# Kernel tuning notes

Measured on AMD Instinct MI355X. Metric: run time of the kernel, lower is better.

Reference implementation:

```python
import jax, jax.numpy as jnp
import numpy as np
from math import sqrt

B, H, L, E = 2, 16, 1024, 64
MEM, LMEM = 896, 128
KV = L + MEM + LMEM  # 2048


def rel_shift(x):
    # Transformer-XL relative shift. x: [B,H,i,j] -> [B,H,i,j]
    b, h, i, j = x.shape
    x = jnp.pad(x, ((0, 0), (0, 0), (0, 0), (0, i)))  # [B,H,i,i+j]
    l = i + j - 1
    x = x.reshape(b, h, -1)
    pad = (-x.shape[-1]) % l
    x = jnp.pad(x, ((0, 0), (0, 0), (0, pad))).reshape(b, h, -1, l)
    return x[..., :i, i - 1:]


def setup_inputs() -> dict:
    key = jax.random.key(0)
    kq, kk, kv_, kp = jax.random.split(key, 4)
    return {
        "q": jax.random.normal(kq, (B, H, L, E), jnp.float32),
        "k": jax.random.normal(kk, (B, H, KV, E), jnp.float32),
        "v": jax.random.normal(kv_, (B, H, KV, E), jnp.float32),
        "attn_mask": jnp.ones((B, L), bool),
        "pos_emb": jax.random.normal(kp, (H, KV, E), jnp.float32),
        "kv_len": KV,
        "mem_len": MEM,
        "lmem_len": LMEM,
    }


def reference(q, k, v, attn_mask, pos_emb, kv_len, mem_len, lmem_len):
    b, h, l, e = q.shape
    scale = 1.0 / sqrt(e)
    dots = jnp.einsum('bhid,bhjd->bhij', q, k) * scale  # [B,H,L,KV]
    mask_value = -jnp.finfo(dots.dtype).max

    # relative position bias
    pos = pos_emb[:, -kv_len:].astype(q.dtype)  # [H,KV,E]
    pos_dots = jnp.einsum('bhid,hjd->bhij', q, pos) * scale
    pos_dots = rel_shift(pos_dots)
    left = dots.shape[-1] - pos_dots.shape[-1]
    pos_dots = jnp.pad(pos_dots, ((0, 0), (0, 0), (0, 0), (left, 0)))
    dots = dots + pos_dots

    total_mem = mem_len + lmem_len
    # padding mask
    m = attn_mask[:, None, :, None] & attn_mask[:, None, None, :]  # [B,1,L,L]
    m = jnp.pad(m, ((0, 0), (0, 0), (0, 0), (total_mem, 0)), constant_values=True)
    dots = jnp.where(m, dots, mask_value)
    # causal mask (memory positions always visible)
    causal = jnp.triu(jnp.ones((l, l + total_mem), bool), k=1 + total_mem)
    dots = jnp.where(causal[None, None], mask_value, dots)

    attn = jax.nn.softmax(dots, axis=-1)  # dropout in eval mode -> identity
    out = jnp.einsum('bhij,bhjd->bhid', attn, v)
    return out.transpose(0, 2, 1, 3).reshape(b, l, h * e)
```

## Files before the change

kernel.cpp:

```cpp
#include <hip/hip_runtime.h>
#include <stdint.h>


typedef __attribute__((ext_vector_type(4))) float f32x4;
typedef __attribute__((ext_vector_type(8))) short s16x8;
typedef __attribute__((ext_vector_type(2))) unsigned int u32x2;
typedef unsigned short ushort_t;

#define L_Q 1024
#define NKV 2048
#define TM  1024
#define NPOS 2176

#define WS_K   0
#define WS_VT  4194304
#define WS_POS 8388608
#define WS_TOTAL_USHORT 10616832
#define WS_NEED_BYTES (WS_TOTAL_USHORT * 2)

#define QS_CONST (0.125f * 1.44269504088896340736f)
#define M_FIXED 8.0f

__device__ __forceinline__ void mfma16(f32x4& c, s16x8 a, s16x8 b) {
  asm("v_mfma_f32_16x16x32_bf16 %0, %1, %2, %0" : "+v"(c) : "v"(a), "v"(b));
}

__device__ __forceinline__ float exp2_(float x) {
#if __has_builtin(__builtin_amdgcn_exp2f)
  return __builtin_amdgcn_exp2f(x);
#else
  float r; asm("v_exp_f32 %0, %1" : "=v"(r) : "v"(x)); return r;
#endif
}

__device__ __forceinline__ ushort_t f2bf(float f) {
  union { float f; unsigned int u; } v; v.f = f;
  unsigned int u = v.u;
  return (ushort_t)((u + 0x7FFFu + ((u >> 16) & 1u)) >> 16);
}

__device__ __forceinline__ void gl_lds16(const ushort_t* g, ushort_t* l) {
  __builtin_amdgcn_global_load_lds(
      (const __attribute__((address_space(1))) unsigned int*)g,
      (__attribute__((address_space(3))) unsigned int*)l, 16, 0, 0);
}

__device__ __forceinline__ s16x8 ldfrag(const ushort_t* base, int row, int chunk) {
  int idx = (row * 64 + chunk * 8) ^ ((row & 7) << 3);
  return *(const s16x8*)(base + idx);
}


#define NK_U 524288
#define NP_U 278528
#define LIN_TOTAL 802816

__global__ __launch_bounds__(256) void prep_lin(
    const float* __restrict__ k, const float* __restrict__ pos,
    ushort_t* __restrict__ ws)
{
  int u = blockIdx.x * 256 + threadIdx.x;
  if (u >= LIN_TOTAL) return;
  if (u < NK_U) {
    int bh = u >> 14, rem = u & 16383;
    int j = rem >> 3, db = (rem & 7) << 3;
    size_t off = (((size_t)(bh << 11) + j) << 6);
    f32x4 a = *(const f32x4*)(k + off + db);
    f32x4 b = *(const f32x4*)(k + off + db + 4);
    s16x8 o;
    o[0] = (short)f2bf(a[0]); o[1] = (short)f2bf(a[1]);
    o[2] = (short)f2bf(a[2]); o[3] = (short)f2bf(a[3]);
    o[4] = (short)f2bf(b[0]); o[5] = (short)f2bf(b[1]);
    o[6] = (short)f2bf(b[2]); o[7] = (short)f2bf(b[3]);
    *(s16x8*)(ws + WS_K + off + (db ^ ((j & 7) << 3))) = o;
  } else {
    int t = u - NK_U;
    int h = t / 17408;
    int rem = t - h * 17408;
    int p = rem >> 3, db = (rem & 7) << 3;
    s16x8 o;
    if (p < 2048) {
      size_t off = (((size_t)(h << 11) + p) << 6) + db;
      f32x4 a = *(const f32x4*)(pos + off);
      f32x4 b = *(const f32x4*)(pos + off + 4);
      o[0] = (short)f2bf(a[0]); o[1] = (short)f2bf(a[1]);
      o[2] = (short)f2bf(a[2]); o[3] = (short)f2bf(a[3]);
      o[4] = (short)f2bf(b[0]); o[5] = (short)f2bf(b[1]);
      o[6] = (short)f2bf(b[2]); o[7] = (short)f2bf(b[3]);
    } else {
      for (int e = 0; e < 8; ++e) o[e] = 0;
    }
    *(s16x8*)(ws + WS_POS + (size_t)h * (NPOS * 64) + p * 64 + (db ^ ((p & 7) << 3))) = o;
  }
}

__global__ __launch_bounds__(256) void prep_vt(
    const float* __restrict__ v, ushort_t* __restrict__ ws)
{
  int u = blockIdx.x * 256 + threadIdx.x;
  int bh = u >> 12, rem = u & 4095;
  int tile = rem >> 7, r2 = rem & 127;
  int jl = r2 >> 3, db = (r2 & 7) << 3;
  int j0 = tile << 6;
  ushort_t vals[4][8];
#pragma unroll
  for (int m = 0; m < 4; ++m) {
    size_t off = (((size_t)(bh << 11) + j0 + jl + 16 * m) << 6) + db;
    f32x4 a = *(const f32x4*)(v + off);
    f32x4 b = *(const f32x4*)(v + off + 4);
    vals[m][0] = f2bf(a[0]); vals[m][1] = f2bf(a[1]);
    vals[m][2] = f2bf(a[2]); vals[m][3] = f2bf(a[3]);
    vals[m][4] = f2bf(b[0]); vals[m][5] = f2bf(b[1]);
    vals[m][6] = f2bf(b[2]); vals[m][7] = f2bf(b[3]);
  }
  ushort_t* vt = ws + WS_VT;
#pragma unroll
  for (int e = 0; e < 8; ++e) {
    int d = db + e;
    int cpos = (jl << 2) ^ ((d & 7) << 3);
    union { ushort_t s[4]; u32x2 w; } pk;
    pk.s[0] = vals[0][e]; pk.s[1] = vals[1][e];
    pk.s[2] = vals[2][e]; pk.s[3] = vals[3][e];
    *(u32x2*)(vt + (((size_t)(bh << 6) + d) << 11) + j0 + cpos) = pk.w;
  }
}


__global__ __launch_bounds__(256, 2) void memattn_fast(
    const float* __restrict__ q, const ushort_t* __restrict__ ws,
    float* __restrict__ out)
{
  __shared__ __align__(16) ushort_t sK[2][64 * 64];
  __shared__ __align__(16) ushort_t sV[2][64 * 64];
  __shared__ __align__(16) ushort_t sPos[2][128 * 64];
  __shared__ __align__(16) ushort_t sPl[4 * 16 * 72];

  const int tid = threadIdx.x;
  const int lane = tid & 63;
  const int w = tid >> 6;
  const int bid = blockIdx.x;
  const int bh = bid & 31;
  const int raw = bid >> 5;
  const int ib = (raw < 8) ? raw : 23 - raw;
  const int h = bh & 15;
  const int b = bh >> 4;
  const int i0 = ib * 64;
  const int iw0 = i0 + w * 16;
  const int jc = lane & 15;
  const int g = lane >> 4;

  const ushort_t* kb = ws + WS_K + (size_t)bh * (NKV * 64);
  const ushort_t* vtb = ws + WS_VT + (size_t)bh * (64 * NKV);
  const ushort_t* pb = ws + WS_POS + (size_t)h * (NPOS * 64);

  s16x8 qf[2];
  {
    const float* qr = q + (size_t)bh * (L_Q * 64) + (size_t)(iw0 + jc) * 64 + g * 8;
#pragma unroll
    for (int c = 0; c < 2; ++c) {
      f32x4 a = *(const f32x4*)(qr + 32 * c);
      f32x4 b2 = *(const f32x4*)(qr + 32 * c + 4);
      s16x8 f;
      f[0] = (short)f2bf(a[0] * QS_CONST); f[1] = (short)f2bf(a[1] * QS_CONST);
      f[2] = (short)f2bf(a[2] * QS_CONST); f[3] = (short)f2bf(a[3] * QS_CONST);
      f[4] = (short)f2bf(b2[0] * QS_CONST); f[5] = (short)f2bf(b2[1] * QS_CONST);
      f[6] = (short)f2bf(b2[2] * QS_CONST); f[7] = (short)f2bf(b2[3] * QS_CONST);
      qf[c] = f;
    }
  }

  f32x4 l4, acc[4];
#pragma unroll
  for (int r = 0; r < 4; ++r) l4[r] = 0.f;
#pragma unroll
  for (int d = 0; d < 4; ++d) { f32x4 z = {0.f, 0.f, 0.f, 0.f}; acc[d] = z; }

  int srcl[4]; int lof[4];
#pragma unroll
  for (int reg = 0; reg < 4; ++reg) {
    int r = 4 * g + reg;
    int sc = jc + 15 - r;
    srcl[reg] = (lane & 48) | (sc & 15);
    lof[reg] = (sc < 16);
  }

  const int nsteps = ib + 17;
  const int lrow8 = lane >> 3;
  const int lc8 = (lane & 7) * 8;

  auto STAGE = [&](int buf, int st) {
    const int j0 = st * 64;
    const int pwb = j0 - i0 + 960;
#pragma unroll
    for (int c2 = 0; c2 < 2; ++c2) {
      int c = 2 * w + c2;
      gl_lds16(kb + (size_t)(j0 + c * 8 + lrow8) * 64 + lc8, &sK[buf][c * 512]);
    }
#pragma unroll
    for (int c2 = 0; c2 < 2; ++c2) {
      int c = 2 * w + c2;
      gl_lds16(vtb + (size_t)(c * 8 + lrow8) * NKV + j0 + lc8, &sV[buf][c * 512]);
    }
#pragma unroll
    for (int c2 = 0; c2 < 4; ++c2) {
      int c = 4 * w + c2;
      gl_lds16(pb + (size_t)(pwb + c * 8 + lrow8) * 64 + lc8, &sPos[buf][c * 512]);
    }
  };

  STAGE(0, 0);
  asm volatile("s_waitcnt vmcnt(0)" ::: "memory");
  __syncthreads();
  int cur = 0;

  for (int st = 0; st < nsteps; ++st) {
    const int j0 = st * 64;
    if (st + 1 < nsteps) STAGE(cur ^ 1, st + 1);

    f32x4 s4[4];
#pragma unroll
    for (int t = 0; t < 4; ++t) {
      f32x4 z = {0.f, 0.f, 0.f, 0.f};
      s4[t] = z;
#pragma unroll
      for (int c = 0; c < 2; ++c)
        mfma16(s4[t], qf[c], ldfrag(sK[cur], 16 * t + jc, g + 4 * c));
    }
    f32x4 pd[5];
#pragma unroll
    for (int t = 0; t < 5; ++t) {
      f32x4 z = {0.f, 0.f, 0.f, 0.f};
      pd[t] = z;
      int lr = 48 - 16 * w + 16 * t + jc;
#pragma unroll
      for (int c = 0; c < 2; ++c)
        mfma16(pd[t], qf[c], ldfrag(sPos[cur], lr, g + 4 * c));
    }
#pragma unroll
    for (int reg = 0; reg < 4; ++reg) {
      float sh0 = __shfl(pd[0][reg], srcl[reg], 64);
      float sh1 = __shfl(pd[1][reg], srcl[reg], 64);
      float sh2 = __shfl(pd[2][reg], srcl[reg], 64);
      float sh3 = __shfl(pd[3][reg], srcl[reg], 64);
      float sh4 = __shfl(pd[4][reg], srcl[reg], 64);
      s4[0][reg] += lof[reg] ? sh0 : sh1;
      s4[1][reg] += lof[reg] ? sh1 : sh2;
      s4[2][reg] += lof[reg] ? sh2 : sh3;
      s4[3][reg] += lof[reg] ? sh3 : sh4;
    }
    if (j0 + 63 - iw0 > TM) {
#pragma unroll
      for (int t = 0; t < 4; ++t)
#pragma unroll
        for (int reg = 0; reg < 4; ++reg) {
          int j = j0 + 16 * t + jc;
          int i = iw0 + 4 * g + reg;
          if (j - i > TM) s4[t][reg] = -1e30f;
        }
    }
    f32x4 ps[4];
#pragma unroll
    for (int reg = 0; reg < 4; ++reg) {
      float rs = 0.f;
#pragma unroll
      for (int t = 0; t < 4; ++t) {
        float pv = exp2_(s4[t][reg] - M_FIXED);
        ps[t][reg] = pv;
        rs += pv;
      }
      l4[reg] += rs;
    }
#pragma unroll
    for (int reg = 0; reg < 4; ++reg) {
      int r = 4 * g + reg;
      unsigned int lo = (unsigned int)f2bf(ps[0][reg]) | ((unsigned int)f2bf(ps[1][reg]) << 16);
      unsigned int hi = (unsigned int)f2bf(ps[2][reg]) | ((unsigned int)f2bf(ps[3][reg]) << 16);
      u32x2 pk2 = {lo, hi};
      *(u32x2*)(sPl + (w * 16 + r) * 72 + jc * 4) = pk2;
    }
    asm volatile("s_waitcnt lgkmcnt(0)" ::: "memory");
#pragma unroll
    for (int kk = 0; kk < 2; ++kk) {
      s16x8 pa = *(const s16x8*)(sPl + (w * 16 + jc) * 72 + 8 * g + 32 * kk);
#pragma unroll
      for (int d = 0; d < 4; ++d)
        mfma16(acc[d], pa, ldfrag(sV[cur], 16 * d + jc, g + 4 * kk));
    }
    asm volatile("s_waitcnt vmcnt(0)" ::: "memory");
    __syncthreads();
    cur ^= 1;
  }

#pragma unroll
  for (int reg = 0; reg < 4; ++reg) {
    float lv = l4[reg];
    lv += __shfl_xor(lv, 1, 16);
    lv += __shfl_xor(lv, 2, 16);
    lv += __shfl_xor(lv, 4, 16);
    lv += __shfl_xor(lv, 8, 16);
    float rinv = 1.0f / lv;
    int i = iw0 + 4 * g + reg;
#pragma unroll
    for (int d = 0; d < 4; ++d) {
      int col = h * 64 + 16 * d + jc;
      out[(size_t)(b * L_Q + i) * 1024 + col] = acc[d][reg] * rinv;
    }
  }
}


__global__ __launch_bounds__(512, 1) void memattn_fallback(
    const float* __restrict__ q, const float* __restrict__ k,
    const float* __restrict__ v, const float* __restrict__ pos,
    float* __restrict__ out)
{
  __shared__ __align__(16) ushort_t sK[64 * 64];
  __shared__ __align__(16) ushort_t sV[64 * 64];
  __shared__ __align__(16) ushort_t sP[256 * 64];
  __shared__ __align__(16) ushort_t sPl[8 * 16 * 72];

  const int tid = threadIdx.x;
  const int lane = tid & 63;
  const int w = tid >> 6;
  const int bid = blockIdx.x;
  const int bh = bid & 31;
  const int ib = bid >> 5;
  const int h = bh & 15;
  const int b = bh >> 4;
  const int i0 = ib * 128;
  const int iw0 = i0 + w * 16;
  const int jc = lane & 15;
  const int g = lane >> 4;

  const float* qb = q + (size_t)bh * L_Q * 64;
  const float* kb = k + (size_t)bh * NKV * 64;
  const float* vb = v + (size_t)bh * NKV * 64;
  const float* pb = pos + (size_t)h * NKV * 64;

  s16x8 qf[2];
  {
    const float* qr = qb + (size_t)(iw0 + jc) * 64 + g * 8;
#pragma unroll
    for (int c = 0; c < 2; ++c) {
      f32x4 a = *(const f32x4*)(qr + 32 * c);
      f32x4 b2 = *(const f32x4*)(qr + 32 * c + 4);
      s16x8 f;
      f[0] = (short)f2bf(a[0] * QS_CONST); f[1] = (short)f2bf(a[1] * QS_CONST);
      f[2] = (short)f2bf(a[2] * QS_CONST); f[3] = (short)f2bf(a[3] * QS_CONST);
      f[4] = (short)f2bf(b2[0] * QS_CONST); f[5] = (short)f2bf(b2[1] * QS_CONST);
      f[6] = (short)f2bf(b2[2] * QS_CONST); f[7] = (short)f2bf(b2[3] * QS_CONST);
      qf[c] = f;
    }
  }

  f32x4 m4, l4, acc[4];
#pragma unroll
  for (int r = 0; r < 4; ++r) { m4[r] = -1e30f; l4[r] = 0.f; }
#pragma unroll
  for (int d = 0; d < 4; ++d) { f32x4 z = {0.f, 0.f, 0.f, 0.f}; acc[d] = z; }

  int srcl[4]; int lof[4];
#pragma unroll
  for (int reg = 0; reg < 4; ++reg) {
    int r = 4 * g + reg;
    int sc = jc + 15 - r;
    srcl[reg] = (lane & 48) | (sc & 15);
    lof[reg] = (sc < 16);
  }

  const int limit = iw0 + 15 + TM;
  const int nsteps = i0 / 64 + 18;
  int staged_hi = 0;

  const int srow = tid >> 3;
  const int c8 = (tid & 7) * 8;

  for (int st = 0; st < nsteps; ++st) {
    const int j0 = st * 64;
    __syncthreads();

    {
      const float* kr = kb + (size_t)(j0 + srow) * 64 + c8;
      f32x4 a = *(const f32x4*)(kr);
      f32x4 b2 = *(const f32x4*)(kr + 4);
      s16x8 fk;
      fk[0] = (short)f2bf(a[0]);  fk[1] = (short)f2bf(a[1]);
      fk[2] = (short)f2bf(a[2]);  fk[3] = (short)f2bf(a[3]);
      fk[4] = (short)f2bf(b2[0]); fk[5] = (short)f2bf(b2[1]);
      fk[6] = (short)f2bf(b2[2]); fk[7] = (short)f2bf(b2[3]);
      int idx = (srow * 64 + c8) ^ ((srow & 7) << 3);
      *(s16x8*)(sK + idx) = fk;

      const float* vr = vb + (size_t)(j0 + srow) * 64 + c8;
      f32x4 va = *(const f32x4*)(vr);
      f32x4 vb2 = *(const f32x4*)(vr + 4);
      float vals[8] = {va[0], va[1], va[2], va[3], vb2[0], vb2[1], vb2[2], vb2[3]};
      int pj = (srow & 15) * 4 + (srow >> 4);
#pragma unroll
      for (int e = 0; e < 8; ++e) {
        int d = c8 + e;
        int vidx = (d * 64 + pj) ^ ((d & 7) << 3);
        sV[vidx] = f2bf(vals[e]);
      }
    }
    {
      int p_lo = (st == 0) ? (896 - i0) : staged_hi;
      int cnt = (st == 0) ? 192 : 64;
      for (int ro = srow; ro < cnt; ro += 64) {
        int p = p_lo + ro;
        int pg = p < 2047 ? p : 2047;
        const float* pr = pb + (size_t)pg * 64 + c8;
        f32x4 a = *(const f32x4*)(pr);
        f32x4 b2 = *(const f32x4*)(pr + 4);
        s16x8 fp;
        fp[0] = (short)f2bf(a[0]);  fp[1] = (short)f2bf(a[1]);
        fp[2] = (short)f2bf(a[2]);  fp[3] = (short)f2bf(a[3]);
        fp[4] = (short)f2bf(b2[0]); fp[5] = (short)f2bf(b2[1]);
        fp[6] = (short)f2bf(b2[2]); fp[7] = (short)f2bf(b2[3]);
        int rr = p & 255;
        int idx = (rr * 64 + c8) ^ ((rr & 7) << 3);
        *(s16x8*)(sP + idx) = fp;
      }
      staged_hi = p_lo + cnt;
    }
    __syncthreads();

    if (j0 > limit) continue;

    f32x4 s4[4];
#pragma unroll
    for (int t = 0; t < 4; ++t) {
      f32x4 z = {0.f, 0.f, 0.f, 0.f};
      s4[t] = z;
#pragma unroll
      for (int c = 0; c < 2; ++c)
        mfma16(s4[t], qf[c], ldfrag(sK, 16 * t + jc, g + 4 * c));
    }
    const int pw0 = j0 - iw0 + 1008;
    f32x4 pd[5];
#pragma unroll
    for (int t = 0; t < 5; ++t) {
      f32x4 z = {0.f, 0.f, 0.f, 0.f};
      pd[t] = z;
      int prow = (pw0 + 16 * t + jc) & 255;
#pragma unroll
      for (int c = 0; c < 2; ++c)
        mfma16(pd[t], qf[c], ldfrag(sP, prow, g + 4 * c));
    }
#pragma unroll
    for (int t = 0; t < 4; ++t) {
#pragma unroll
      for (int reg = 0; reg < 4; ++reg) {
        float a0 = __shfl(pd[t][reg], srcl[reg], 64);
        float a1 = __shfl(pd[t + 1][reg], srcl[reg], 64);
        s4[t][reg] += lof[reg] ? a0 : a1;
      }
    }
    if (j0 + 63 - iw0 > TM) {
#pragma unroll
      for (int t = 0; t < 4; ++t)
#pragma unroll
        for (int reg = 0; reg < 4; ++reg) {
          int j = j0 + 16 * t + jc;
          int i = iw0 + 4 * g + reg;
          if (j - i > TM) s4[t][reg] = -1e30f;
        }
    }
    f32x4 ps[4];
#pragma unroll
    for (int reg = 0; reg < 4; ++reg) {
      float mx = fmaxf(fmaxf(s4[0][reg], s4[1][reg]), fmaxf(s4[2][reg], s4[3][reg]));
      mx = fmaxf(mx, __shfl_xor(mx, 1, 16));
      mx = fmaxf(mx, __shfl_xor(mx, 2, 16));
      mx = fmaxf(mx, __shfl_xor(mx, 4, 16));
      mx = fmaxf(mx, __shfl_xor(mx, 8, 16));
      float mold = m4[reg];
      float mnew = fmaxf(mold, mx);
      float sf = exp2_(mold - mnew);
      m4[reg] = mnew;
      float rs = 0.f;
#pragma unroll
      for (int t = 0; t < 4; ++t) {
        float pv = exp2_(s4[t][reg] - mnew);
        ps[t][reg] = pv;
        rs += pv;
      }
      l4[reg] = l4[reg] * sf + rs;
#pragma unroll
      for (int d = 0; d < 4; ++d) acc[d][reg] *= sf;
    }
#pragma unroll
    for (int reg = 0; reg < 4; ++reg) {
      int r = 4 * g + reg;
      unsigned int lo = (unsigned int)f2bf(ps[0][reg]) | ((unsigned int)f2bf(ps[1][reg]) << 16);
      unsigned int hi = (unsigned int)f2bf(ps[2][reg]) | ((unsigned int)f2bf(ps[3][reg]) << 16);
      u32x2 pk2 = {lo, hi};
      *(u32x2*)(sPl + (w * 16 + r) * 72 + jc * 4) = pk2;
    }
    asm volatile("s_waitcnt lgkmcnt(0)" ::: "memory");
#pragma unroll
    for (int kk = 0; kk < 2; ++kk) {
      s16x8 pa = *(const s16x8*)(sPl + (w * 16 + jc) * 72 + 8 * g + 32 * kk);
#pragma unroll
      for (int d = 0; d < 4; ++d)
        mfma16(acc[d], pa, ldfrag(sV, 16 * d + jc, g + 4 * kk));
    }
  }

#pragma unroll
  for (int reg = 0; reg < 4; ++reg) {
    float lv = l4[reg];
    lv += __shfl_xor(lv, 1, 16);
    lv += __shfl_xor(lv, 2, 16);
    lv += __shfl_xor(lv, 4, 16);
    lv += __shfl_xor(lv, 8, 16);
    float rinv = 1.0f / lv;
    int i = iw0 + 4 * g + reg;
#pragma unroll
    for (int d = 0; d < 4; ++d) {
      int col = h * 64 + 16 * d + jc;
      out[(size_t)(b * L_Q + i) * 1024 + col] = acc[d][reg] * rinv;
    }
  }
}

extern "C" void kernel_launch(void* const* d_in, const int* in_sizes, int n_in,
                              void* d_out, int out_size, void* d_ws, size_t ws_size,
                              hipStream_t stream) {
  (void)in_sizes; (void)n_in; (void)out_size;
  const float* q = (const float*)d_in[0];
  const float* k = (const float*)d_in[1];
  const float* v = (const float*)d_in[2];
  const float* pos = (const float*)d_in[4];
  float* out = (float*)d_out;

  if (ws_size >= (size_t)WS_NEED_BYTES) {
    ushort_t* ws = (ushort_t*)d_ws;
    hipLaunchKernelGGL(prep_lin, dim3((LIN_TOTAL + 255) / 256), dim3(256), 0, stream,
                       k, pos, ws);
    hipLaunchKernelGGL(prep_vt, dim3(512), dim3(256), 0, stream, v, ws);
    hipLaunchKernelGGL(memattn_fast, dim3(512), dim3(256), 0, stream, q, ws, out);
  } else {
    hipLaunchKernelGGL(memattn_fallback, dim3(256), dim3(512), 0, stream,
                       q, k, v, pos, out);
  }
}
```

Before: 72.76 us.

## Process two query sub-tiles per wave and ring-buffer positional rows

Each block now runs two waves instead of four, and each wave handles two 16-row query tiles, so every K, V and positional fragment read from LDS feeds two MFMAs. The positional window moves from a double-buffered 128-row tile to a 192-row ring buffer that only loads 64 new rows per step, reusing the overlapping rows between consecutive steps. This cuts LDS reads and global positional traffic per output. In exchange there are half as many waves per block, which lowers latency hiding, and register pressure is higher.

```diff
diff --git a/kernel.cpp b/kernel.cpp
--- a/kernel.cpp
+++ b/kernel.cpp
@@ -126,14 +126,14 @@
 }
 
 
-__global__ __launch_bounds__(256, 2) void memattn_fast(
+__global__ __launch_bounds__(128, 1) void memattn_fast(
     const float* __restrict__ q, const ushort_t* __restrict__ ws,
     float* __restrict__ out)
 {
   __shared__ __align__(16) ushort_t sK[2][64 * 64];
   __shared__ __align__(16) ushort_t sV[2][64 * 64];
-  __shared__ __align__(16) ushort_t sPos[2][128 * 64];
-  __shared__ __align__(16) ushort_t sPl[4 * 16 * 72];
+  __shared__ __align__(16) ushort_t sPos[192 * 64];
+  __shared__ __align__(16) ushort_t sPl[64 * 72];
 
   const int tid = threadIdx.x;
   const int lane = tid & 63;
@@ -145,7 +145,8 @@
   const int h = bh & 15;
   const int b = bh >> 4;
   const int i0 = ib * 64;
-  const int iw0 = i0 + w * 16;
+  const int iwA = i0 + (2 * w + 0) * 16;
+  const int iwB = i0 + (2 * w + 1) * 16;
   const int jc = lane & 15;
   const int g = lane >> 4;
 
@@ -153,9 +154,11 @@
   const ushort_t* vtb = ws + WS_VT + (size_t)bh * (64 * NKV);
   const ushort_t* pb = ws + WS_POS + (size_t)h * (NPOS * 64);
 
-  s16x8 qf[2];
-  {
-    const float* qr = q + (size_t)bh * (L_Q * 64) + (size_t)(iw0 + jc) * 64 + g * 8;
+  s16x8 qfA[2], qfB[2];
+#pragma unroll
+  for (int s = 0; s < 2; ++s) {
+    const int iw = s ? iwB : iwA;
+    const float* qr = q + (size_t)bh * (L_Q * 64) + (size_t)(iw + jc) * 64 + g * 8;
 #pragma unroll
     for (int c = 0; c < 2; ++c) {
       f32x4 a = *(const f32x4*)(qr + 32 * c);
@@ -165,15 +168,18 @@
       f[2] = (short)f2bf(a[2] * QS_CONST); f[3] = (short)f2bf(a[3] * QS_CONST);
       f[4] = (short)f2bf(b2[0] * QS_CONST); f[5] = (short)f2bf(b2[1] * QS_CONST);
       f[6] = (short)f2bf(b2[2] * QS_CONST); f[7] = (short)f2bf(b2[3] * QS_CONST);
-      qf[c] = f;
-    }
-  }
-
-  f32x4 l4, acc[4];
-#pragma unroll
-  for (int r = 0; r < 4; ++r) l4[r] = 0.f;
-#pragma unroll
-  for (int d = 0; d < 4; ++d) { f32x4 z = {0.f, 0.f, 0.f, 0.f}; acc[d] = z; }
+      if (s) qfB[c] = f; else qfA[c] = f;
+    }
+  }
+
+  f32x4 l4A, l4B, accA[4], accB[4];
+#pragma unroll
+  for (int r = 0; r < 4; ++r) { l4A[r] = 0.f; l4B[r] = 0.f; }
+#pragma unroll
+  for (int d = 0; d < 4; ++d) {
+    f32x4 z = {0.f, 0.f, 0.f, 0.f};
+    accA[d] = z; accB[d] = z;
+  }
 
   int srcl[4]; int lof[4];
 #pragma unroll
@@ -187,123 +193,184 @@
   const int nsteps = ib + 17;
   const int lrow8 = lane >> 3;
   const int lc8 = (lane & 7) * 8;
-
-  auto STAGE = [&](int buf, int st) {
+  const int B0 = 960 - i0;
+  const int lrB = 32 - 32 * w + jc;
+
+  auto STAGE_KV = [&](int buf, int st) {
     const int j0 = st * 64;
-    const int pwb = j0 - i0 + 960;
-#pragma unroll
-    for (int c2 = 0; c2 < 2; ++c2) {
-      int c = 2 * w + c2;
-      gl_lds16(kb + (size_t)(j0 + c * 8 + lrow8) * 64 + lc8, &sK[buf][c * 512]);
-    }
-#pragma unroll
-    for (int c2 = 0; c2 < 2; ++c2) {
-      int c = 2 * w + c2;
-      gl_lds16(vtb + (size_t)(c * 8 + lrow8) * NKV + j0 + lc8, &sV[buf][c * 512]);
-    }
 #pragma unroll
     for (int c2 = 0; c2 < 4; ++c2) {
       int c = 4 * w + c2;
-      gl_lds16(pb + (size_t)(pwb + c * 8 + lrow8) * 64 + lc8, &sPos[buf][c * 512]);
+      gl_lds16(kb + (size_t)(j0 + c * 8 + lrow8) * 64 + lc8, &sK[buf][c * 512]);
+    }
+#pragma unroll
+    for (int c2 = 0; c2 < 4; ++c2) {
+      int c = 4 * w + c2;
+      gl_lds16(vtb + (size_t)(c * 8 + lrow8) * NKV + j0 + lc8, &sV[buf][c * 512]);
     }
   };
-
-  STAGE(0, 0);
+  auto STAGE_P = [&](int st, int rbase) {
+    const int abs0 = B0 + st * 64 + 128;
+#pragma unroll
+    for (int c2 = 0; c2 < 4; ++c2) {
+      int c = 4 * w + c2;
+      int rdest = rbase + 128 + c * 8;
+      if (rdest >= 192) rdest -= 192;
+      gl_lds16(pb + (size_t)(abs0 + c * 8 + lrow8) * 64 + lc8, &sPos[rdest * 64]);
+    }
+  };
+
+  int rb = B0 % 192;
+  STAGE_KV(0, 0);
+#pragma unroll
+  for (int c2 = 0; c2 < 8; ++c2) {
+    int c = 8 * w + c2;
+    int rdest = rb + c * 8;
+    if (rdest >= 192) rdest -= 192;
+    gl_lds16(pb + (size_t)(B0 + c * 8 + lrow8) * 64 + lc8, &sPos[rdest * 64]);
+  }
   asm volatile("s_waitcnt vmcnt(0)" ::: "memory");
   __syncthreads();
   int cur = 0;
 
   for (int st = 0; st < nsteps; ++st) {
     const int j0 = st * 64;
-    if (st + 1 < nsteps) STAGE(cur ^ 1, st + 1);
-
-    f32x4 s4[4];
+    if (st + 1 < nsteps) {
+      STAGE_KV(cur ^ 1, st + 1);
+      STAGE_P(st, rb);
+    }
+
+    f32x4 sA[4], sB[4];
 #pragma unroll
     for (int t = 0; t < 4; ++t) {
       f32x4 z = {0.f, 0.f, 0.f, 0.f};
-      s4[t] = z;
-#pragma unroll
-      for (int c = 0; c < 2; ++c)
-        mfma16(s4[t], qf[c], ldfrag(sK[cur], 16 * t + jc, g + 4 * c));
-    }
-    f32x4 pd[5];
+      sA[t] = z; sB[t] = z;
+#pragma unroll
+      for (int c = 0; c < 2; ++c) {
+        s16x8 kf = ldfrag(sK[cur], 16 * t + jc, g + 4 * c);
+        mfma16(sA[t], qfA[c], kf);
+        mfma16(sB[t], qfB[c], kf);
+      }
+    }
+    f32x4 pdA[5], pdB[5];
 #pragma unroll
     for (int t = 0; t < 5; ++t) {
       f32x4 z = {0.f, 0.f, 0.f, 0.f};
-      pd[t] = z;
-      int lr = 48 - 16 * w + 16 * t + jc;
-#pragma unroll
-      for (int c = 0; c < 2; ++c)
-        mfma16(pd[t], qf[c], ldfrag(sPos[cur], lr, g + 4 * c));
+      pdA[t] = z; pdB[t] = z;
+    }
+#pragma unroll
+    for (int tp = 0; tp < 6; ++tp) {
+      int rr = rb + lrB + 16 * tp;
+      if (rr >= 192) rr -= 192;
+#pragma unroll
+      for (int c = 0; c < 2; ++c) {
+        s16x8 pf = ldfrag(sPos, rr, g + 4 * c);
+        if (tp >= 1) mfma16(pdA[tp - 1], qfA[c], pf);
+        if (tp <= 4) mfma16(pdB[tp], qfB[c], pf);
+      }
     }
 #pragma unroll
     for (int reg = 0; reg < 4; ++reg) {
-      float sh0 = __shfl(pd[0][reg], srcl[reg], 64);
-      float sh1 = __shfl(pd[1][reg], srcl[reg], 64);
-      float sh2 = __shfl(pd[2][reg], srcl[reg], 64);
-      float sh3 = __shfl(pd[3][reg], srcl[reg], 64);
-      float sh4 = __shfl(pd[4][reg], srcl[reg], 64);
-      s4[0][reg] += lof[reg] ? sh0 : sh1;
-      s4[1][reg] += lof[reg] ? sh1 : sh2;
-      s4[2][reg] += lof[reg] ? sh2 : sh3;
-      s4[3][reg] += lof[reg] ? sh3 : sh4;
-    }
-    if (j0 + 63 - iw0 > TM) {
+      float a0 = __shfl(pdA[0][reg], srcl[reg], 64);
+      float a1 = __shfl(pdA[1][reg], srcl[reg], 64);
+      float a2 = __shfl(pdA[2][reg], srcl[reg], 64);
+      float a3 = __shfl(pdA[3][reg], srcl[reg], 64);
+      float a4 = __shfl(pdA[4][reg], srcl[reg], 64);
+      sA[0][reg] += lof[reg] ? a0 : a1;
+      sA[1][reg] += lof[reg] ? a1 : a2;
+      sA[2][reg] += lof[reg] ? a2 : a3;
+      sA[3][reg] += lof[reg] ? a3 : a4;
+      float b0 = __shfl(pdB[0][reg], srcl[reg], 64);
+      float b1 = __shfl(pdB[1][reg], srcl[reg], 64);
+      float b2 = __shfl(pdB[2][reg], srcl[reg], 64);
+      float b3 = __shfl(pdB[3][reg], srcl[reg], 64);
+      float b4 = __shfl(pdB[4][reg], srcl[reg], 64);
+      sB[0][reg] += lof[reg] ? b0 : b1;
+      sB[1][reg] += lof[reg] ? b1 : b2;
+      sB[2][reg] += lof[reg] ? b2 : b3;
+      sB[3][reg] += lof[reg] ? b3 : b4;
+    }
+    if (j0 + 63 - iwA > TM) {
 #pragma unroll
       for (int t = 0; t < 4; ++t)
 #pragma unroll
         for (int reg = 0; reg < 4; ++reg) {
           int j = j0 + 16 * t + jc;
-          int i = iw0 + 4 * g + reg;
-          if (j - i > TM) s4[t][reg] = -1e30f;
+          int i = iwA + 4 * g + reg;
+          if (j - i > TM) sA[t][reg] = -1e30f;
         }
     }
-    f32x4 ps[4];
+    if (j0 + 63 - iwB > TM) {
+#pragma unroll
+      for (int t = 0; t < 4; ++t)
+#pragma unroll
+        for (int reg = 0; reg < 4; ++reg) {
+          int j = j0 + 16 * t + jc;
+          int i = iwB + 4 * g + reg;
+          if (j - i > TM) sB[t][reg] = -1e30f;
+        }
+    }
+    f32x4 psA[4], psB[4];
 #pragma unroll
     for (int reg = 0; reg < 4; ++reg) {
-      float rs = 0.f;
+      float rsA = 0.f, rsB = 0.f;
 #pragma unroll
       for (int t = 0; t < 4; ++t) {
-        float pv = exp2_(s4[t][reg] - M_FIXED);
-        ps[t][reg] = pv;
-        rs += pv;
-      }
-      l4[reg] += rs;
+        float pa = exp2_(sA[t][reg] - M_FIXED);
+        float pbv = exp2_(sB[t][reg] - M_FIXED);
+        psA[t][reg] = pa; psB[t][reg] = pbv;
+        rsA += pa; rsB += pbv;
+      }
+      l4A[reg] += rsA; l4B[reg] += rsB;
     }
 #pragma unroll
     for (int reg = 0; reg < 4; ++reg) {
       int r = 4 * g + reg;
-      unsigned int lo = (unsigned int)f2bf(ps[0][reg]) | ((unsigned int)f2bf(ps[1][reg]) << 16);
-      unsigned int hi = (unsigned int)f2bf(ps[2][reg]) | ((unsigned int)f2bf(ps[3][reg]) << 16);
-      u32x2 pk2 = {lo, hi};
-      *(u32x2*)(sPl + (w * 16 + r) * 72 + jc * 4) = pk2;
+      unsigned int loA = (unsigned int)f2bf(psA[0][reg]) | ((unsigned int)f2bf(psA[1][reg]) << 16);
+      unsigned int hiA = (unsigned int)f2bf(psA[2][reg]) | ((unsigned int)f2bf(psA[3][reg]) << 16);
+      u32x2 pkA = {loA, hiA};
+      *(u32x2*)(sPl + ((2 * w) * 16 + r) * 72 + jc * 4) = pkA;
+      unsigned int loB = (unsigned int)f2bf(psB[0][reg]) | ((unsigned int)f2bf(psB[1][reg]) << 16);
+      unsigned int hiB = (unsigned int)f2bf(psB[2][reg]) | ((unsigned int)f2bf(psB[3][reg]) << 16);
+      u32x2 pkB = {loB, hiB};
+      *(u32x2*)(sPl + ((2 * w + 1) * 16 + r) * 72 + jc * 4) = pkB;
     }
     asm volatile("s_waitcnt lgkmcnt(0)" ::: "memory");
 #pragma unroll
     for (int kk = 0; kk < 2; ++kk) {
-      s16x8 pa = *(const s16x8*)(sPl + (w * 16 + jc) * 72 + 8 * g + 32 * kk);
-#pragma unroll
-      for (int d = 0; d < 4; ++d)
-        mfma16(acc[d], pa, ldfrag(sV[cur], 16 * d + jc, g + 4 * kk));
+      s16x8 paA = *(const s16x8*)(sPl + ((2 * w) * 16 + jc) * 72 + 8 * g + 32 * kk);
+      s16x8 paB = *(const s16x8*)(sPl + ((2 * w + 1) * 16 + jc) * 72 + 8 * g + 32 * kk);
+#pragma unroll
+      for (int d = 0; d < 4; ++d) {
+        s16x8 vf = ldfrag(sV[cur], 16 * d + jc, g + 4 * kk);
+        mfma16(accA[d], paA, vf);
+        mfma16(accB[d], paB, vf);
+      }
     }
     asm volatile("s_waitcnt vmcnt(0)" ::: "memory");
     __syncthreads();
     cur ^= 1;
-  }
-
-#pragma unroll
-  for (int reg = 0; reg < 4; ++reg) {
-    float lv = l4[reg];
-    lv += __shfl_xor(lv, 1, 16);
-    lv += __shfl_xor(lv, 2, 16);
-    lv += __shfl_xor(lv, 4, 16);
-    lv += __shfl_xor(lv, 8, 16);
-    float rinv = 1.0f / lv;
-    int i = iw0 + 4 * g + reg;
-#pragma unroll
-    for (int d = 0; d < 4; ++d) {
-      int col = h * 64 + 16 * d + jc;
-      out[(size_t)(b * L_Q + i) * 1024 + col] = acc[d][reg] * rinv;
+    rb += 64; if (rb >= 192) rb -= 192;
+  }
+
+#pragma unroll
+  for (int s = 0; s < 2; ++s) {
+    const int iw = s ? iwB : iwA;
+#pragma unroll
+    for (int reg = 0; reg < 4; ++reg) {
+      float lv = s ? l4B[reg] : l4A[reg];
+      lv += __shfl_xor(lv, 1, 16);
+      lv += __shfl_xor(lv, 2, 16);
+      lv += __shfl_xor(lv, 4, 16);
+      lv += __shfl_xor(lv, 8, 16);
+      float rinv = 1.0f / lv;
+      int i = iw + 4 * g + reg;
+#pragma unroll
+      for (int d = 0; d < 4; ++d) {
+        int col = h * 64 + 16 * d + jc;
+        float av = s ? accB[d][reg] : accA[d][reg];
+        out[(size_t)(b * L_Q + i) * 1024 + col] = av * rinv;
+      }
     }
   }
 }
@@ -539,7 +606,7 @@
     hipLaunchKernelGGL(prep_lin, dim3((LIN_TOTAL + 255) / 256), dim3(256), 0, stream,
                        k, pos, ws);
     hipLaunchKernelGGL(prep_vt, dim3(512), dim3(256), 0, stream, v, ws);
-    hipLaunchKernelGGL(memattn_fast, dim3(512), dim3(256), 0, stream, q, ws, out);
+    hipLaunchKernelGGL(memattn_fast, dim3(512), dim3(128), 0, stream, q, ws, out);
   } else {
     hipLaunchKernelGGL(memattn_fallback, dim3(256), dim3(512), 0, stream,
                        q, k, v, pos, out);
```

Measured after the change: 93.03 us. 27.9% more time.

## Ring-buffer positional tiles in LDS and reuse overlapping pos-dot tile across steps

Applied to the files above, without the earlier changes.

The positional-embedding window slides by 64 rows per KV step while each step reads 128 rows. The double-buffered 128-row pos tile is replaced by a 192-row ring buffer, so only 64 new rows are fetched per step instead of 128. The last pos-dot MFMA tile of one step is carried into the next step as its first tile, saving two MFMAs per step. The two prep kernels are also merged into one launch. This cuts global traffic and launch overhead but adds modular row indexing and a dependency on ring-slot timing relative to the barrier.

```diff
diff --git a/kernel.cpp b/kernel.cpp
--- a/kernel.cpp
+++ b/kernel.cpp
@@ -53,14 +53,15 @@
 
 #define NK_U 524288
 #define NP_U 278528
-#define LIN_TOTAL 802816
-
-__global__ __launch_bounds__(256) void prep_lin(
+#define NV_U 131072
+#define PREP_TOTAL (NK_U + NP_U + NV_U)
+
+__global__ __launch_bounds__(256) void prep_all(
     const float* __restrict__ k, const float* __restrict__ pos,
-    ushort_t* __restrict__ ws)
+    const float* __restrict__ v, ushort_t* __restrict__ ws)
 {
   int u = blockIdx.x * 256 + threadIdx.x;
-  if (u >= LIN_TOTAL) return;
+  if (u >= PREP_TOTAL) return;
   if (u < NK_U) {
     int bh = u >> 14, rem = u & 16383;
     int j = rem >> 3, db = (rem & 7) << 3;
@@ -73,7 +74,7 @@
     o[4] = (short)f2bf(b[0]); o[5] = (short)f2bf(b[1]);
     o[6] = (short)f2bf(b[2]); o[7] = (short)f2bf(b[3]);
     *(s16x8*)(ws + WS_K + off + (db ^ ((j & 7) << 3))) = o;
-  } else {
+  } else if (u < NK_U + NP_U) {
     int t = u - NK_U;
     int h = t / 17408;
     int rem = t - h * 17408;
@@ -91,37 +92,33 @@
       for (int e = 0; e < 8; ++e) o[e] = 0;
     }
     *(s16x8*)(ws + WS_POS + (size_t)h * (NPOS * 64) + p * 64 + (db ^ ((p & 7) << 3))) = o;
-  }
-}
-
-__global__ __launch_bounds__(256) void prep_vt(
-    const float* __restrict__ v, ushort_t* __restrict__ ws)
-{
-  int u = blockIdx.x * 256 + threadIdx.x;
-  int bh = u >> 12, rem = u & 4095;
-  int tile = rem >> 7, r2 = rem & 127;
-  int jl = r2 >> 3, db = (r2 & 7) << 3;
-  int j0 = tile << 6;
-  ushort_t vals[4][8];
-#pragma unroll
-  for (int m = 0; m < 4; ++m) {
-    size_t off = (((size_t)(bh << 11) + j0 + jl + 16 * m) << 6) + db;
-    f32x4 a = *(const f32x4*)(v + off);
-    f32x4 b = *(const f32x4*)(v + off + 4);
-    vals[m][0] = f2bf(a[0]); vals[m][1] = f2bf(a[1]);
-    vals[m][2] = f2bf(a[2]); vals[m][3] = f2bf(a[3]);
-    vals[m][4] = f2bf(b[0]); vals[m][5] = f2bf(b[1]);
-    vals[m][6] = f2bf(b[2]); vals[m][7] = f2bf(b[3]);
-  }
-  ushort_t* vt = ws + WS_VT;
-#pragma unroll
-  for (int e = 0; e < 8; ++e) {
-    int d = db + e;
-    int cpos = (jl << 2) ^ ((d & 7) << 3);
-    union { ushort_t s[4]; u32x2 w; } pk;
-    pk.s[0] = vals[0][e]; pk.s[1] = vals[1][e];
-    pk.s[2] = vals[2][e]; pk.s[3] = vals[3][e];
-    *(u32x2*)(vt + (((size_t)(bh << 6) + d) << 11) + j0 + cpos) = pk.w;
+  } else {
+    int u2 = u - (NK_U + NP_U);
+    int bh = u2 >> 12, rem = u2 & 4095;
+    int tile = rem >> 7, r2 = rem & 127;
+    int jl = r2 >> 3, db = (r2 & 7) << 3;
+    int j0 = tile << 6;
+    ushort_t vals[4][8];
+#pragma unroll
+    for (int m = 0; m < 4; ++m) {
+      size_t off = (((size_t)(bh << 11) + j0 + jl + 16 * m) << 6) + db;
+      f32x4 a = *(const f32x4*)(v + off);
+      f32x4 b = *(const f32x4*)(v + off + 4);
+      vals[m][0] = f2bf(a[0]); vals[m][1] = f2bf(a[1]);
+      vals[m][2] = f2bf(a[2]); vals[m][3] = f2bf(a[3]);
+      vals[m][4] = f2bf(b[0]); vals[m][5] = f2bf(b[1]);
+      vals[m][6] = f2bf(b[2]); vals[m][7] = f2bf(b[3]);
+    }
+    ushort_t* vt = ws + WS_VT;
+#pragma unroll
+    for (int e = 0; e < 8; ++e) {
+      int d = db + e;
+      int cpos = (jl << 2) ^ ((d & 7) << 3);
+      union { ushort_t s[4]; u32x2 w; } pk;
+      pk.s[0] = vals[0][e]; pk.s[1] = vals[1][e];
+      pk.s[2] = vals[2][e]; pk.s[3] = vals[3][e];
+      *(u32x2*)(vt + (((size_t)(bh << 6) + d) << 11) + j0 + cpos) = pk.w;
+    }
   }
 }
 
@@ -132,7 +129,7 @@
 {
   __shared__ __align__(16) ushort_t sK[2][64 * 64];
   __shared__ __align__(16) ushort_t sV[2][64 * 64];
-  __shared__ __align__(16) ushort_t sPos[2][128 * 64];
+  __shared__ __align__(16) ushort_t sPos[192 * 64];
   __shared__ __align__(16) ushort_t sPl[4 * 16 * 72];
 
   const int tid = threadIdx.x;
@@ -187,10 +184,11 @@
   const int nsteps = ib + 17;
   const int lrow8 = lane >> 3;
   const int lc8 = (lane & 7) * 8;
-
-  auto STAGE = [&](int buf, int st) {
+  const int B0 = 960 - i0;
+  const int lr0 = 48 - 16 * w + jc;
+
+  auto STAGE_KV = [&](int buf, int st) {
     const int j0 = st * 64;
-    const int pwb = j0 - i0 + 960;
 #pragma unroll
     for (int c2 = 0; c2 < 2; ++c2) {
       int c = 2 * w + c2;
@@ -201,21 +199,48 @@
       int c = 2 * w + c2;
       gl_lds16(vtb + (size_t)(c * 8 + lrow8) * NKV + j0 + lc8, &sV[buf][c * 512]);
     }
-#pragma unroll
-    for (int c2 = 0; c2 < 4; ++c2) {
-      int c = 4 * w + c2;
-      gl_lds16(pb + (size_t)(pwb + c * 8 + lrow8) * 64 + lc8, &sPos[buf][c * 512]);
-    }
   };
-
-  STAGE(0, 0);
+  auto STAGE_P = [&](int st, int rbase) {
+    const int abs0 = B0 + st * 64 + 128;
+#pragma unroll
+    for (int c2 = 0; c2 < 2; ++c2) {
+      int c = 2 * w + c2;
+      int rdest = rbase + 128 + c * 8;
+      if (rdest >= 192) rdest -= 192;
+      gl_lds16(pb + (size_t)(abs0 + c * 8 + lrow8) * 64 + lc8, &sPos[rdest * 64]);
+    }
+  };
+
+  int rb = B0 % 192;
+  STAGE_KV(0, 0);
+#pragma unroll
+  for (int c2 = 0; c2 < 4; ++c2) {
+    int c = 4 * w + c2;
+    int rdest = rb + c * 8;
+    if (rdest >= 192) rdest -= 192;
+    gl_lds16(pb + (size_t)(B0 + c * 8 + lrow8) * 64 + lc8, &sPos[rdest * 64]);
+  }
   asm volatile("s_waitcnt vmcnt(0)" ::: "memory");
   __syncthreads();
   int cur = 0;
 
+  f32x4 pdc;
+  {
+    f32x4 z = {0.f, 0.f, 0.f, 0.f};
+    pdc = z;
+    int rr = rb + lr0;
+    if (rr >= 192) rr -= 192;
+#pragma unroll
+    for (int c = 0; c < 2; ++c)
+      mfma16(pdc, qf[c], ldfrag(sPos, rr, g + 4 * c));
+  }
+
   for (int st = 0; st < nsteps; ++st) {
     const int j0 = st * 64;
-    if (st + 1 < nsteps) STAGE(cur ^ 1, st + 1);
+    if (st + 1 < nsteps) {
+      STAGE_KV(cur ^ 1, st + 1);
+      STAGE_P(st, rb);
+    }
 
     f32x4 s4[4];
 #pragma unroll
@@ -227,15 +252,18 @@
         mfma16(s4[t], qf[c], ldfrag(sK[cur], 16 * t + jc, g + 4 * c));
     }
     f32x4 pd[5];
-#pragma unroll
-    for (int t = 0; t < 5; ++t) {
+    pd[0] = pdc;
+#pragma unroll
+    for (int t = 1; t < 5; ++t) {
       f32x4 z = {0.f, 0.f, 0.f, 0.f};
       pd[t] = z;
-      int lr = 48 - 16 * w + 16 * t + jc;
+      int rr = rb + lr0 + 16 * t;
+      if (rr >= 192) rr -= 192;
 #pragma unroll
       for (int c = 0; c < 2; ++c)
-        mfma16(pd[t], qf[c], ldfrag(sPos[cur], lr, g + 4 * c));
-    }
+        mfma16(pd[t], qf[c], ldfrag(sPos, rr, g + 4 * c));
+    }
+    pdc = pd[4];
 #pragma unroll
     for (int reg = 0; reg < 4; ++reg) {
       float sh0 = __shfl(pd[0][reg], srcl[reg], 64);
@@ -289,6 +317,7 @@
     asm volatile("s_waitcnt vmcnt(0)" ::: "memory");
     __syncthreads();
     cur ^= 1;
+    rb += 64; if (rb >= 192) rb -= 192;
   }
 
 #pragma unroll
@@ -536,9 +565,8 @@
 
   if (ws_size >= (size_t)WS_NEED_BYTES) {
     ushort_t* ws = (ushort_t*)d_ws;
-    hipLaunchKernelGGL(prep_lin, dim3((LIN_TOTAL + 255) / 256), dim3(256), 0, stream,
-                       k, pos, ws);
-    hipLaunchKernelGGL(prep_vt, dim3(512), dim3(256), 0, stream, v, ws);
+    hipLaunchKernelGGL(prep_all, dim3((PREP_TOTAL + 255) / 256), dim3(256), 0, stream,
+                       k, pos, v, ws);
     hipLaunchKernelGGL(memattn_fast, dim3(512), dim3(256), 0, stream, q, ws, out);
   } else {
     hipLaunchKernelGGL(memattn_fallback, dim3(256), dim3(512), 0, stream,
```

After: 72.71 us. About the same (-0.1%).
